# Optimization experiments

Hardware: AMD Instinct MI355X
Metric: run time of the kernel (lower is better)

The kernel has to match this reference:

```python
import jax, jax.numpy as jnp
import numpy as np

NUM_LEVELS = 16
FEATURES_PER_LEVEL = 2
LOG2_HASHMAP_SIZE = 19
BASE_RES = 16
FINEST_RES = 2048
N_POINTS = 2097152

_growth = np.exp((np.log(FINEST_RES) - np.log(BASE_RES)) / (NUM_LEVELS - 1))
RESOLUTIONS = np.floor(BASE_RES * _growth ** np.arange(NUM_LEVELS)).astype(np.int64)  # (L,)
TABLE_SIZES = np.minimum(RESOLUTIONS ** 3, 2 ** LOG2_HASHMAP_SIZE).astype(np.int32)   # (L,)
MAX_TABLE_SIZE = 2 ** LOG2_HASHMAP_SIZE

P1, P2, P3 = 73856093, 19349663, 83492791  # spatial hash primes


def setup_inputs() -> dict:
    key = jax.random.key(0)
    k1, k2 = jax.random.split(key)
    coordinates = jax.random.uniform(k1, (N_POINTS, 3), dtype=jnp.float32)
    # keras 'uniform' initializer = U(-0.05, 0.05); tables stacked & zero-padded to max size
    hash_tables = jax.random.uniform(
        k2, (NUM_LEVELS, MAX_TABLE_SIZE, FEATURES_PER_LEVEL),
        minval=-0.05, maxval=0.05, dtype=jnp.float32)
    return {"coordinates": coordinates, "hash_tables": hash_tables}


def reference(coordinates, hash_tables):
    batch_shape = coordinates.shape[:-1]
    coords = coordinates.reshape(-1, 3)  # (N, 3)
    res = jnp.asarray(RESOLUTIONS.astype(np.float32))          # (L,)
    sizes = jnp.asarray(TABLE_SIZES)                            # (L,) int32
    # all levels at once: (L, N, 3)
    grid = jnp.floor(coords[None, :, :] * res[:, None, None]).astype(jnp.int32)
    x, y, t = grid[..., 0], grid[..., 1], grid[..., 2]
    h = (x * np.int32(P1)) ^ (y * np.int32(P2)) ^ (t * np.int32(P3))  # int32 wraparound, like TF
    idx = jnp.abs(h) % sizes[:, None]                           # (L, N)
    feats = jnp.take_along_axis(hash_tables, idx[:, :, None], axis=1)  # (L, N, F)
    out = jnp.transpose(feats, (1, 0, 2)).reshape(coords.shape[0], NUM_LEVELS * FEATURES_PER_LEVEL)
    return out.reshape(*batch_shape, NUM_LEVELS * FEATURES_PER_LEVEL)
```

## Files before the change

### kernel.cpp

```cpp
#include <hip/hip_runtime.h>
#include <hip/hip_fp16.h>
#include <stdint.h>


#define TPB 256

typedef float vfloat4 __attribute__((ext_vector_type(4)));
typedef float vfloat2 __attribute__((ext_vector_type(2)));

__device__ __forceinline__ uint32_t hash_idx(float cx, float cy, float cz,
                                             int resi, int siz)
{
    const float rf = (float)resi;
    const int x = (int)floorf(cx * rf);
    const int y = (int)floorf(cy * rf);
    const int z = (int)floorf(cz * rf);
    const uint32_t h = (uint32_t)x * 73856093u
                     ^ (uint32_t)y * 19349663u
                     ^ (uint32_t)z * 83492791u;
    const int32_t hs = (int32_t)h;
    if (siz == (1 << 19)) {
        const uint32_t a = (hs < 0) ? (0u - h) : h;
        return a & 0x7FFFFu;
    } else {
        int32_t a = (hs < 0) ? (int32_t)(0u - h) : hs;
        int32_t r = a % siz;
        if (r < 0) r += siz;
        return (uint32_t)r;
    }
}

__device__ __forceinline__ uint32_t pack_h2(float a, float b)
{
    const __half ha = __float2half_rn(a);
    const __half hb = __float2half_rn(b);
    return (uint32_t)__half_as_ushort(ha)
         | ((uint32_t)__half_as_ushort(hb) << 16);
}

__device__ __forceinline__ vfloat2 unpack_h2(uint32_t v)
{
    vfloat2 r;
    r.x = __half2float(__ushort_as_half((uint16_t)(v & 0xFFFFu)));
    r.y = __half2float(__ushort_as_half((uint16_t)(v >> 16)));
    return r;
}

#define RESI_LIST {16, 22, 30, 42, 58, 80, 111, 153, \
                   212, 294, 406, 561, 776, 1072, 1482, 2048}
#define SIZ_LIST  {4096, 10648, 27000, 74088, 195112, 512000, \
                   524288, 524288, 524288, 524288, 524288, \
                   524288, 524288, 524288, 524288, 524288}

template<int LV>
__device__ __forceinline__ void gather_body(
    const float* __restrict__ coords,
    const float* __restrict__ tables,
    uint32_t* __restrict__ ws,
    int npts, long long pb, int t)
{
    constexpr int RESI[16] = RESI_LIST;
    constexpr int SIZ[16] = SIZ_LIST;

    const long long base = pb * 2048;
    const float* tab = tables + ((size_t)LV << 20);

    uint32_t g[8];
#pragma unroll
    for (int j = 0; j < 8; ++j) {
        const long long p = base + j * 256 + t;
        const float cx = coords[3 * p + 0];
        const float cy = coords[3 * p + 1];
        const float cz = coords[3 * p + 2];
        const uint32_t idx = hash_idx(cx, cy, cz, RESI[LV], SIZ[LV]);
        const vfloat2 f = *reinterpret_cast<const vfloat2*>(
            tab + ((size_t)idx << 1));
        g[j] = pack_h2(f.x, f.y);
    }
    uint32_t* wl = ws + (size_t)(LV - 5) * npts + base;
#pragma unroll
    for (int j = 0; j < 8; ++j)
        __builtin_nontemporal_store(g[j], wl + j * 256 + t);
}

__global__ __launch_bounds__(TPB) void hashenc_gather_merged(
    const float* __restrict__ coords,
    const float* __restrict__ tables,
    uint32_t* __restrict__ ws,
    int npts)
{
    const int t = threadIdx.x;
    const int c = blockIdx.x & 7;
    const long long k = blockIdx.x >> 3;
    const long long npb = (long long)npts >> 11;

    if (k < npb) {
        switch (c) {
            case 0: gather_body<5>(coords, tables, ws, npts, k, t); break;
            case 1: gather_body<6>(coords, tables, ws, npts, k, t); break;
            case 2: gather_body<7>(coords, tables, ws, npts, k, t); break;
            case 3: gather_body<8>(coords, tables, ws, npts, k, t); break;
            case 4: gather_body<9>(coords, tables, ws, npts, k, t); break;
            case 5: gather_body<10>(coords, tables, ws, npts, k, t); break;
            case 6: gather_body<11>(coords, tables, ws, npts, k, t); break;
            case 7: gather_body<12>(coords, tables, ws, npts, k, t); break;
        }
    } else {
        const long long per_class = (3 * npb + 7) >> 3;
        const long long ti = (long long)c * per_class + (k - npb);
        if (ti < 3 * npb) {
            const long long pb = ti % npb;
            switch ((int)(ti / npb)) {
                case 0: gather_body<13>(coords, tables, ws, npts, pb, t); break;
                case 1: gather_body<14>(coords, tables, ws, npts, pb, t); break;
                case 2: gather_body<15>(coords, tables, ws, npts, pb, t); break;
            }
        }
    }
}

__global__ __launch_bounds__(TPB) void hashenc_transpose_fused(
    const float* __restrict__ coords,
    const float* __restrict__ tables,
    const uint32_t* __restrict__ ws,
    float* __restrict__ out,
    int npts)
{
    constexpr int RESI[16] = RESI_LIST;
    constexpr int SIZ[16] = SIZ_LIST;

    __shared__ float buf[128 * 33];

    const int t = threadIdx.x;
    const long long pbase = (long long)blockIdx.x * TPB;
    const long long p = pbase + t;

    const float cx = coords[3 * p + 0];
    const float cy = coords[3 * p + 1];
    const float cz = coords[3 * p + 2];

    vfloat2 feat[16];
#pragma unroll
    for (int l = 0; l < 5; ++l) {
        const uint32_t idx = hash_idx(cx, cy, cz, RESI[l], SIZ[l]);
        feat[l] = *reinterpret_cast<const vfloat2*>(
            tables + ((size_t)l << 20) + ((size_t)idx << 1));
    }
#pragma unroll
    for (int l = 5; l < 16; ++l) {
        const uint32_t v = __builtin_nontemporal_load(
            ws + (size_t)(l - 5) * npts + p);
        feat[l] = unpack_h2(v);
    }

    float* oblk = out + pbase * 32;
#pragma unroll
    for (int h = 0; h < 2; ++h) {
        if ((t >> 7) == h) {
            const int r = t & 127;
#pragma unroll
            for (int l = 0; l < 16; ++l) {
                buf[r * 33 + 2 * l + 0] = feat[l].x;
                buf[r * 33 + 2 * l + 1] = feat[l].y;
            }
        }
        __syncthreads();
#pragma unroll
        for (int k = 0; k < 4; ++k) {
            const int f = k * 1024 + t * 4;
            const int row = f >> 5;
            const int col = f & 31;
            const vfloat4 v = *reinterpret_cast<const vfloat4*>(&buf[row * 33 + col]);
            __builtin_nontemporal_store(v,
                reinterpret_cast<vfloat4*>(&oblk[(long long)h * 4096 + f]));
        }
        __syncthreads();
    }
}

__global__ __launch_bounds__(TPB) void hashenc_kernel(
    const float* __restrict__ coords,
    const float* __restrict__ tables,
    float* __restrict__ out,
    int npts)
{
    constexpr int RESI[16] = RESI_LIST;
    constexpr int SIZ[16] = SIZ_LIST;

    __shared__ float buf[128 * 33];

    const int t = threadIdx.x;
    const long long pbase = (long long)blockIdx.x * TPB;
    const long long p = pbase + t;

    const float cx = coords[3 * p + 0];
    const float cy = coords[3 * p + 1];
    const float cz = coords[3 * p + 2];

    float2 feat[16];
#pragma unroll
    for (int l = 0; l < 16; ++l) {
        const uint32_t idx = hash_idx(cx, cy, cz, RESI[l], SIZ[l]);
        feat[l] = *reinterpret_cast<const float2*>(
            tables + ((size_t)l << 20) + ((size_t)idx << 1));
    }

    float* oblk = out + pbase * 32;
#pragma unroll
    for (int h = 0; h < 2; ++h) {
        if ((t >> 7) == h) {
            const int r = t & 127;
#pragma unroll
            for (int l = 0; l < 16; ++l) {
                buf[r * 33 + 2 * l + 0] = feat[l].x;
                buf[r * 33 + 2 * l + 1] = feat[l].y;
            }
        }
        __syncthreads();
#pragma unroll
        for (int k = 0; k < 4; ++k) {
            const int f = k * 1024 + t * 4;
            const int row = f >> 5;
            const int col = f & 31;
            const vfloat4 v = *reinterpret_cast<const vfloat4*>(&buf[row * 33 + col]);
            __builtin_nontemporal_store(v,
                reinterpret_cast<vfloat4*>(&oblk[(long long)h * 4096 + f]));
        }
        __syncthreads();
    }
}

extern "C" void kernel_launch(void* const* d_in, const int* in_sizes, int n_in,
                              void* d_out, int out_size, void* d_ws, size_t ws_size,
                              hipStream_t stream)
{
    const float* coords = (const float*)d_in[0];
    const float* tables = (const float*)d_in[1];
    float* out = (float*)d_out;
    const int npts = in_sizes[0] / 3;

    const size_t need = (size_t)11 * (size_t)npts * sizeof(uint32_t);
    if (ws_size >= need && (npts % 2048) == 0) {
        uint32_t* ws = (uint32_t*)d_ws;
        const long long npb = npts / 2048;
        const long long per_class = (3 * npb + 7) / 8;
        const dim3 g((unsigned)(8 * (npb + per_class))), b(TPB);
        hipLaunchKernelGGL(hashenc_gather_merged, g, b, 0, stream,
                           coords, tables, ws, npts);
        hipLaunchKernelGGL(hashenc_transpose_fused, dim3(npts / TPB), b, 0, stream,
                           coords, tables, (const uint32_t*)d_ws, out, npts);
    } else {
        hipLaunchKernelGGL(hashenc_kernel, dim3(npts / TPB), dim3(TPB), 0, stream,
                           coords, tables, out, npts);
    }
}
```

Measured before the change: 273.8 us.

## Software-pipeline gather and transpose stages across point slices in one kernel

```diff
diff --git a/kernel.cpp b/kernel.cpp
--- a/kernel.cpp
+++ b/kernel.cpp
@@ -83,48 +83,12 @@
         __builtin_nontemporal_store(g[j], wl + j * 256 + t);
 }
 
-__global__ __launch_bounds__(TPB) void hashenc_gather_merged(
+__global__ __launch_bounds__(TPB) void hashenc_pipe(
     const float* __restrict__ coords,
     const float* __restrict__ tables,
     uint32_t* __restrict__ ws,
-    int npts)
-{
-    const int t = threadIdx.x;
-    const int c = blockIdx.x & 7;
-    const long long k = blockIdx.x >> 3;
-    const long long npb = (long long)npts >> 11;
-
-    if (k < npb) {
-        switch (c) {
-            case 0: gather_body<5>(coords, tables, ws, npts, k, t); break;
-            case 1: gather_body<6>(coords, tables, ws, npts, k, t); break;
-            case 2: gather_body<7>(coords, tables, ws, npts, k, t); break;
-            case 3: gather_body<8>(coords, tables, ws, npts, k, t); break;
-            case 4: gather_body<9>(coords, tables, ws, npts, k, t); break;
-            case 5: gather_body<10>(coords, tables, ws, npts, k, t); break;
-            case 6: gather_body<11>(coords, tables, ws, npts, k, t); break;
-            case 7: gather_body<12>(coords, tables, ws, npts, k, t); break;
-        }
-    } else {
-        const long long per_class = (3 * npb + 7) >> 3;
-        const long long ti = (long long)c * per_class + (k - npb);
-        if (ti < 3 * npb) {
-            const long long pb = ti % npb;
-            switch ((int)(ti / npb)) {
-                case 0: gather_body<13>(coords, tables, ws, npts, pb, t); break;
-                case 1: gather_body<14>(coords, tables, ws, npts, pb, t); break;
-                case 2: gather_body<15>(coords, tables, ws, npts, pb, t); break;
-            }
-        }
-    }
-}
-
-__global__ __launch_bounds__(TPB) void hashenc_transpose_fused(
-    const float* __restrict__ coords,
-    const float* __restrict__ tables,
-    const uint32_t* __restrict__ ws,
     float* __restrict__ out,
-    int npts)
+    int npts, int gs, int ts, int gblocks, int npb_s)
 {
     constexpr int RESI[16] = RESI_LIST;
     constexpr int SIZ[16] = SIZ_LIST;
@@ -132,7 +96,41 @@
     __shared__ float buf[128 * 33];
 
     const int t = threadIdx.x;
-    const long long pbase = (long long)blockIdx.x * TPB;
+
+    if ((int)blockIdx.x < gblocks) {
+        const int c = blockIdx.x & 7;
+        const long long k = blockIdx.x >> 3;
+        const long long off = (long long)gs * npb_s;
+
+        if (k < npb_s) {
+            const long long pb = off + k;
+            switch (c) {
+                case 0: gather_body<5>(coords, tables, ws, npts, pb, t); break;
+                case 1: gather_body<6>(coords, tables, ws, npts, pb, t); break;
+                case 2: gather_body<7>(coords, tables, ws, npts, pb, t); break;
+                case 3: gather_body<8>(coords, tables, ws, npts, pb, t); break;
+                case 4: gather_body<9>(coords, tables, ws, npts, pb, t); break;
+                case 5: gather_body<10>(coords, tables, ws, npts, pb, t); break;
+                case 6: gather_body<11>(coords, tables, ws, npts, pb, t); break;
+                case 7: gather_body<12>(coords, tables, ws, npts, pb, t); break;
+            }
+        } else {
+            const long long per_class = (3LL * npb_s + 7) >> 3;
+            const long long ti = (long long)c * per_class + (k - npb_s);
+            if (ti < 3LL * npb_s) {
+                const long long pb = off + ti % npb_s;
+                switch ((int)(ti / npb_s)) {
+                    case 0: gather_body<13>(coords, tables, ws, npts, pb, t); break;
+                    case 1: gather_body<14>(coords, tables, ws, npts, pb, t); break;
+                    case 2: gather_body<15>(coords, tables, ws, npts, pb, t); break;
+                }
+            }
+        }
+        return;
+    }
+
+    const int tb = (int)blockIdx.x - gblocks;
+    const long long pbase = ((long long)ts * npb_s * 8 + tb) * 256;
     const long long p = pbase + t;
 
     const float cx = coords[3 * p + 0];
@@ -239,16 +237,22 @@
     float* out = (float*)d_out;
     const int npts = in_sizes[0] / 3;
 
+    const int S = 4;
     const size_t need = (size_t)11 * (size_t)npts * sizeof(uint32_t);
-    if (ws_size >= need && (npts % 2048) == 0) {
+    if (ws_size >= need && (npts % (2048 * S)) == 0) {
         uint32_t* ws = (uint32_t*)d_ws;
-        const long long npb = npts / 2048;
-        const long long per_class = (3 * npb + 7) / 8;
-        const dim3 g((unsigned)(8 * (npb + per_class))), b(TPB);
-        hipLaunchKernelGGL(hashenc_gather_merged, g, b, 0, stream,
-                           coords, tables, ws, npts);
-        hipLaunchKernelGGL(hashenc_transpose_fused, dim3(npts / TPB), b, 0, stream,
-                           coords, tables, (const uint32_t*)d_ws, out, npts);
+        const int npb_s = npts / 2048 / S;
+        const int per_class_s = (3 * npb_s + 7) / 8;
+        const int gblocks = 8 * (npb_s + per_class_s);
+        const int tblocks = npb_s * 8;
+        for (int i = 0; i <= S; ++i) {
+            const int gs = (i < S) ? i : -1;
+            const int ts = i - 1;
+            const int gb = (gs >= 0) ? gblocks : 0;
+            const int tb = (ts >= 0) ? tblocks : 0;
+            hipLaunchKernelGGL(hashenc_pipe, dim3(gb + tb), dim3(TPB), 0, stream,
+                               coords, tables, ws, out, npts, gs, ts, gb, npb_s);
+        }
     } else {
         hipLaunchKernelGGL(hashenc_kernel, dim3(npts / TPB), dim3(TPB), 0, stream,
                            coords, tables, out, npts);
```

After: 302.7 us. +10.6%, slower.
